# Optimization experiments

Measured on AMD Instinct MI355X. Metric: run time of the kernel, lower is better.

## Reference

```python
import jax, jax.numpy as jnp
import numpy as np

B, N_LATENT, N_NUISANCE, N_OUT = 2048, 64, 16, 2048


def setup_inputs() -> dict:
    key = jax.random.key(0)
    ks = jax.random.split(key, 6)
    z = jax.random.normal(ks[0], (B, N_LATENT + N_NUISANCE), dtype=jnp.float32)
    size_factor = jax.random.uniform(ks[1], (B, 1), dtype=jnp.float32) + 0.5
    # nn.Linear(n_latent, n_out, bias=False): store as [L, O] for z0 @ W
    amat_w = jax.random.normal(ks[2], (N_LATENT, N_OUT), dtype=jnp.float32) / np.sqrt(N_LATENT).astype(np.float32)
    amat_site = jax.random.normal(ks[3], (N_NUISANCE, N_LATENT, N_OUT), dtype=jnp.float32)
    offsets = jax.random.normal(ks[4], (N_NUISANCE, N_OUT), dtype=jnp.float32)
    px_r = jax.random.normal(ks[5], (N_OUT,), dtype=jnp.float32)
    return {"z": z, "size_factor": size_factor, "amat_w": amat_w,
            "amat_site": amat_site, "offsets": offsets, "px_r": px_r}


def reference(z, size_factor, amat_w, amat_site, offsets, px_r):
    n_nuisance = offsets.shape[0]
    nuisance_oh = z[..., -n_nuisance:]          # [B, N] one-hot site indicator
    z0 = z[..., :-n_nuisance]                   # [B, L] latent part
    x1 = z0 @ amat_w                            # [B, O] shared linear decoder
    nuisance_ids = jnp.argmax(nuisance_oh, axis=-1)  # [B] int ids
    # dropout(p=0.1) in eval mode == identity; .detach() -> stop_gradient
    z0_d = jax.lax.stop_gradient(z0)
    As = amat_site[nuisance_ids]                # [B, L, O] per-sample gathered weights
    x2 = jnp.einsum('bl,blo->bo', z0_d, As)     # batched matvec reduction over L
    mu = jax.nn.softmax(x1 + x2 + offsets[nuisance_ids], axis=-1)  # [B, O]
    mu = mu * size_factor                       # scale by per-cell size factor
    theta = jnp.exp(px_r)                       # NB inverse-dispersion, [O]
    return mu, theta
```

## Files before the change

kernel.cpp:

```cpp
#include <hip/hip_runtime.h>
#include <hip/hip_bf16.h>

#define NB 2048
#define NL 64
#define NN 16
#define NROW 80
#define NO 2048
#define TPB 256
#define OPT 8

typedef unsigned int   u32;
typedef unsigned short u16;

__device__ __forceinline__ float bflo(u32 u) { union { u32 i; float f; } c; c.i = u << 16;          return c.f; }
__device__ __forceinline__ float bfhi(u32 u) { union { u32 i; float f; } c; c.i = u & 0xffff0000u;  return c.f; }
__device__ __forceinline__ u16 f2bf(float f) { __hip_bfloat16 h = __float2bfloat16(f); return *(u16*)&h; }

__global__ __launch_bounds__(TPB) void build_m(const float* __restrict__ W,
                                               const float* __restrict__ A,
                                               u16* __restrict__ M) {
    size_t t    = (size_t)blockIdx.x * TPB + threadIdx.x;
    size_t base = t * 4;
    float4 w = *(const float4*)(W + (base & (size_t)(NL * NO - 1)));
    float4 a = *(const float4*)(A + base);
    ushort4 m;
    m.x = f2bf(w.x + a.x);
    m.y = f2bf(w.y + a.y);
    m.z = f2bf(w.z + a.z);
    m.w = f2bf(w.w + a.w);
    *(ushort4*)(M + base) = m;
}

__global__ __launch_bounds__(TPB) void decoder_m(
    const float* __restrict__ z,
    const float* __restrict__ sf,
    const u16*   __restrict__ M,
    const float* __restrict__ offs,
    const float* __restrict__ pxr,
    float* __restrict__ out)
{
    const int b   = blockIdx.x;
    const int tid = threadIdx.x;

    if (b == NB) {
        for (int o = tid; o < NO; o += TPB)
            out[(size_t)NB * NO + o] = __expf(pxr[o]);
        return;
    }

    __shared__ float z0s[NL];
    __shared__ int   s_id;
    __shared__ float s_red[6];

    if (tid < NL) z0s[tid] = z[b * NROW + tid];
    if (tid == 0) {
        float best = -1e30f; int bi = 0;
        for (int i = 0; i < NN; ++i) {
            float v = z[b * NROW + NL + i];
            if (v > best) { best = v; bi = i; }
        }
        s_id = bi;
    }
    __syncthreads();
    const int id = s_id;

    const int o0 = tid * OPT;
    const uint4* mv = (const uint4*)(M + (size_t)id * NL * NO + o0);

    float acc[OPT];
    {
        float4 oa = *(const float4*)(offs + id * NO + o0);
        float4 ob = *(const float4*)(offs + id * NO + o0 + 4);
        acc[0] = oa.x; acc[1] = oa.y; acc[2] = oa.z; acc[3] = oa.w;
        acc[4] = ob.x; acc[5] = ob.y; acc[6] = ob.z; acc[7] = ob.w;
    }

    #pragma unroll 8
    for (int l = 0; l < NL; ++l) {
        const float zl = z0s[l];
        uint4 m = mv[l * (NO / OPT)];
        acc[0] += zl * bflo(m.x); acc[1] += zl * bfhi(m.x);
        acc[2] += zl * bflo(m.y); acc[3] += zl * bfhi(m.y);
        acc[4] += zl * bflo(m.z); acc[5] += zl * bfhi(m.z);
        acc[6] += zl * bflo(m.w); acc[7] += zl * bfhi(m.w);
    }

    float m = acc[0];
    #pragma unroll
    for (int j = 1; j < OPT; ++j) m = fmaxf(m, acc[j]);
    #pragma unroll
    for (int off = 32; off > 0; off >>= 1) m = fmaxf(m, __shfl_down(m, off));
    if ((tid & 63) == 0) s_red[tid >> 6] = m;
    __syncthreads();
    if (tid == 0) s_red[4] = fmaxf(fmaxf(s_red[0], s_red[1]), fmaxf(s_red[2], s_red[3]));
    __syncthreads();
    const float mx = s_red[4];

    float ex[OPT];
    float s = 0.f;
    #pragma unroll
    for (int j = 0; j < OPT; ++j) { ex[j] = __expf(acc[j] - mx); s += ex[j]; }
    #pragma unroll
    for (int off = 32; off > 0; off >>= 1) s += __shfl_down(s, off);
    if ((tid & 63) == 0) s_red[tid >> 6] = s;
    __syncthreads();
    if (tid == 0) s_red[5] = (s_red[0] + s_red[1]) + (s_red[2] + s_red[3]);
    __syncthreads();
    const float scale = sf[b] / s_red[5];

    float* op = out + (size_t)b * NO + o0;
    *(float4*)(op)     = make_float4(ex[0] * scale, ex[1] * scale, ex[2] * scale, ex[3] * scale);
    *(float4*)(op + 4) = make_float4(ex[4] * scale, ex[5] * scale, ex[6] * scale, ex[7] * scale);
}

__global__ __launch_bounds__(TPB) void decoder_f(
    const float* __restrict__ z, const float* __restrict__ sf,
    const float* __restrict__ W, const float* __restrict__ A,
    const float* __restrict__ offs, const float* __restrict__ pxr,
    float* __restrict__ out)
{
    const int b   = blockIdx.x;
    const int tid = threadIdx.x;
    if (b == NB) {
        for (int o = tid; o < NO; o += TPB)
            out[(size_t)NB * NO + o] = __expf(pxr[o]);
        return;
    }
    __shared__ float z0s[NL];
    __shared__ int   s_id;
    __shared__ float s_red[6];
    if (tid < NL) z0s[tid] = z[b * NROW + tid];
    if (tid == 0) {
        float best = -1e30f; int bi = 0;
        for (int i = 0; i < NN; ++i) {
            float v = z[b * NROW + NL + i];
            if (v > best) { best = v; bi = i; }
        }
        s_id = bi;
    }
    __syncthreads();
    const int id = s_id;
    const int o0 = tid * OPT;
    const float* wp = W + o0;
    const float* ap = A + (size_t)id * NL * NO + o0;
    float acc[OPT];
    {
        float4 oa = *(const float4*)(offs + id * NO + o0);
        float4 ob = *(const float4*)(offs + id * NO + o0 + 4);
        acc[0] = oa.x; acc[1] = oa.y; acc[2] = oa.z; acc[3] = oa.w;
        acc[4] = ob.x; acc[5] = ob.y; acc[6] = ob.z; acc[7] = ob.w;
    }
    #pragma unroll 4
    for (int l = 0; l < NL; ++l) {
        const float zl = z0s[l];
        float4 w0 = *(const float4*)(wp + l * NO);
        float4 w1 = *(const float4*)(wp + l * NO + 4);
        float4 a0 = *(const float4*)(ap + l * NO);
        float4 a1 = *(const float4*)(ap + l * NO + 4);
        acc[0] += zl * (w0.x + a0.x); acc[1] += zl * (w0.y + a0.y);
        acc[2] += zl * (w0.z + a0.z); acc[3] += zl * (w0.w + a0.w);
        acc[4] += zl * (w1.x + a1.x); acc[5] += zl * (w1.y + a1.y);
        acc[6] += zl * (w1.z + a1.z); acc[7] += zl * (w1.w + a1.w);
    }
    float m = acc[0];
    #pragma unroll
    for (int j = 1; j < OPT; ++j) m = fmaxf(m, acc[j]);
    #pragma unroll
    for (int off = 32; off > 0; off >>= 1) m = fmaxf(m, __shfl_down(m, off));
    if ((tid & 63) == 0) s_red[tid >> 6] = m;
    __syncthreads();
    if (tid == 0) s_red[4] = fmaxf(fmaxf(s_red[0], s_red[1]), fmaxf(s_red[2], s_red[3]));
    __syncthreads();
    const float mx = s_red[4];
    float ex[OPT];
    float s = 0.f;
    #pragma unroll
    for (int j = 0; j < OPT; ++j) { ex[j] = __expf(acc[j] - mx); s += ex[j]; }
    #pragma unroll
    for (int off = 32; off > 0; off >>= 1) s += __shfl_down(s, off);
    if ((tid & 63) == 0) s_red[tid >> 6] = s;
    __syncthreads();
    if (tid == 0) s_red[5] = (s_red[0] + s_red[1]) + (s_red[2] + s_red[3]);
    __syncthreads();
    const float scale = sf[b] / s_red[5];
    float* op = out + (size_t)b * NO + o0;
    *(float4*)(op)     = make_float4(ex[0] * scale, ex[1] * scale, ex[2] * scale, ex[3] * scale);
    *(float4*)(op + 4) = make_float4(ex[4] * scale, ex[5] * scale, ex[6] * scale, ex[7] * scale);
}

extern "C" void kernel_launch(void* const* d_in, const int* in_sizes, int n_in,
                              void* d_out, int out_size, void* d_ws, size_t ws_size,
                              hipStream_t stream) {
    const float* z    = (const float*)d_in[0];
    const float* sf   = (const float*)d_in[1];
    const float* W    = (const float*)d_in[2];
    const float* A    = (const float*)d_in[3];
    const float* offs = (const float*)d_in[4];
    const float* pxr  = (const float*)d_in[5];
    float* out = (float*)d_out;

    const size_t m_bytes = (size_t)NN * NL * NO * sizeof(u16);
    if (ws_size >= m_bytes) {
        u16* M = (u16*)d_ws;
        hipLaunchKernelGGL(build_m, dim3((NN * NL * NO / 4) / TPB), dim3(TPB), 0, stream, W, A, M);
        hipLaunchKernelGGL(decoder_m, dim3(NB + 1), dim3(TPB), 0, stream, z, sf, M, offs, pxr, out);
    } else {
        hipLaunchKernelGGL(decoder_f, dim3(NB + 1), dim3(TPB), 0, stream, z, sf, W, A, offs, pxr, out);
    }
}
```

Measured before the change: 101.8 us.

## Bucket rows by nuisance id and process groups of eight rows per block

A prep kernel now computes each row's argmax site id, builds per-site row lists with shared-memory atomics, and also does the bf16 weight fold and the theta exp. The decoder launches one block per chunk of eight same-site rows, so each bf16 weight tile load is reused across eight rows instead of one. This cuts weight traffic per output row but raises register pressure (64 accumulators per thread) and launches many empty blocks for sparse buckets. Row order within a bucket depends on atomics, which does not change the results.

```diff
diff --git a/kernel.cpp b/kernel.cpp
--- a/kernel.cpp
+++ b/kernel.cpp
@@ -8,6 +8,9 @@
 #define NO 2048
 #define TPB 256
 #define OPT 8
+#define G 8
+#define CHUNKS (NB / G)
+#define MBLK (NN * NL * NO / 4 / TPB)
 
 typedef unsigned int   u32;
 typedef unsigned short u16;
@@ -16,101 +19,170 @@
 __device__ __forceinline__ float bfhi(u32 u) { union { u32 i; float f; } c; c.i = u & 0xffff0000u;  return c.f; }
 __device__ __forceinline__ u16 f2bf(float f) { __hip_bfloat16 h = __float2bfloat16(f); return *(u16*)&h; }
 
-__global__ __launch_bounds__(TPB) void build_m(const float* __restrict__ W,
-                                               const float* __restrict__ A,
-                                               u16* __restrict__ M) {
-    size_t t    = (size_t)blockIdx.x * TPB + threadIdx.x;
-    size_t base = t * 4;
-    float4 w = *(const float4*)(W + (base & (size_t)(NL * NO - 1)));
-    float4 a = *(const float4*)(A + base);
-    ushort4 m;
-    m.x = f2bf(w.x + a.x);
-    m.y = f2bf(w.y + a.y);
-    m.z = f2bf(w.z + a.z);
-    m.w = f2bf(w.w + a.w);
-    *(ushort4*)(M + base) = m;
-}
-
-__global__ __launch_bounds__(TPB) void decoder_m(
+__global__ __launch_bounds__(TPB) void prep(
+    const float* __restrict__ W,
+    const float* __restrict__ A,
+    const float* __restrict__ z,
+    const float* __restrict__ pxr,
+    u16* __restrict__ M,
+    u32* __restrict__ counts,
+    u32* __restrict__ perm,
+    float* __restrict__ out)
+{
+    const int blk = blockIdx.x;
+    const int tid = threadIdx.x;
+
+    if (blk < MBLK) {
+        size_t t    = (size_t)blk * TPB + tid;
+        size_t base = t * 4;
+        float4 w = *(const float4*)(W + (base & (size_t)(NL * NO - 1)));
+        float4 a = *(const float4*)(A + base);
+        ushort4 m;
+        m.x = f2bf(w.x + a.x);
+        m.y = f2bf(w.y + a.y);
+        m.z = f2bf(w.z + a.z);
+        m.w = f2bf(w.w + a.w);
+        *(ushort4*)(M + base) = m;
+        return;
+    }
+
+    if (blk == MBLK) {
+        __shared__ u32 lc[NN];
+        if (tid < NN) lc[tid] = 0;
+        __syncthreads();
+        #pragma unroll
+        for (int k = 0; k < NB / TPB; ++k) {
+            const int b = k * TPB + tid;
+            const float* zp = z + (size_t)b * NROW + NL;
+            float4 v0 = *(const float4*)(zp);
+            float4 v1 = *(const float4*)(zp + 4);
+            float4 v2 = *(const float4*)(zp + 8);
+            float4 v3 = *(const float4*)(zp + 12);
+            float best = v0.x; int bi = 0;
+            #define CK(val, idx) if ((val) > best) { best = (val); bi = (idx); }
+            CK(v0.y, 1)  CK(v0.z, 2)  CK(v0.w, 3)
+            CK(v1.x, 4)  CK(v1.y, 5)  CK(v1.z, 6)  CK(v1.w, 7)
+            CK(v2.x, 8)  CK(v2.y, 9)  CK(v2.z, 10) CK(v2.w, 11)
+            CK(v3.x, 12) CK(v3.y, 13) CK(v3.z, 14) CK(v3.w, 15)
+            #undef CK
+            u32 pos = atomicAdd(&lc[bi], 1u);
+            perm[(u32)bi * NB + pos] = (u32)b;
+        }
+        __syncthreads();
+        if (tid < NN) counts[tid] = lc[tid];
+        return;
+    }
+
+    for (int o = tid; o < NO; o += TPB)
+        out[(size_t)NB * NO + o] = __expf(pxr[o]);
+}
+
+__global__ __launch_bounds__(TPB) void decoder_g(
     const float* __restrict__ z,
     const float* __restrict__ sf,
     const u16*   __restrict__ M,
     const float* __restrict__ offs,
-    const float* __restrict__ pxr,
+    const u32*   __restrict__ counts,
+    const u32*   __restrict__ perm,
     float* __restrict__ out)
 {
-    const int b   = blockIdx.x;
+    const int bucket = blockIdx.x / CHUNKS;
+    const int chunk  = blockIdx.x % CHUNKS;
+    const u32 cnt    = counts[bucket];
+    if ((u32)(chunk * G) >= cnt) return;
     const int tid = threadIdx.x;
 
-    if (b == NB) {
-        for (int o = tid; o < NO; o += TPB)
-            out[(size_t)NB * NO + o] = __expf(pxr[o]);
-        return;
-    }
-
-    __shared__ float z0s[NL];
-    __shared__ int   s_id;
-    __shared__ float s_red[6];
-
-    if (tid < NL) z0s[tid] = z[b * NROW + tid];
-    if (tid == 0) {
-        float best = -1e30f; int bi = 0;
-        for (int i = 0; i < NN; ++i) {
-            float v = z[b * NROW + NL + i];
-            if (v > best) { best = v; bi = i; }
-        }
-        s_id = bi;
-    }
-    __syncthreads();
-    const int id = s_id;
+    __shared__ float zt[NL][G];
+    __shared__ float s_sf[G];
+    __shared__ u32   s_rows[G];
+    __shared__ float s_red[2][G][4];
+
+    if (tid < G) {
+        u32 idx = (u32)(chunk * G + tid);
+        u32 clamped = idx < cnt ? idx : (cnt - 1u);
+        u32 r = perm[(size_t)bucket * NB + clamped];
+        s_rows[tid] = r;
+        s_sf[tid]   = sf[r];
+    }
+    __syncthreads();
+    {
+        const int l = tid & (NL - 1);
+        const int g = tid >> 6;
+        u32 r0 = s_rows[g], r1 = s_rows[g + 4];
+        zt[l][g]     = z[(size_t)r0 * NROW + l];
+        zt[l][g + 4] = z[(size_t)r1 * NROW + l];
+    }
+    __syncthreads();
 
     const int o0 = tid * OPT;
-    const uint4* mv = (const uint4*)(M + (size_t)id * NL * NO + o0);
-
-    float acc[OPT];
+    const uint4* mv = (const uint4*)(M + (size_t)bucket * (NL * NO) + o0);
+
+    float acc[G][OPT];
     {
-        float4 oa = *(const float4*)(offs + id * NO + o0);
-        float4 ob = *(const float4*)(offs + id * NO + o0 + 4);
-        acc[0] = oa.x; acc[1] = oa.y; acc[2] = oa.z; acc[3] = oa.w;
-        acc[4] = ob.x; acc[5] = ob.y; acc[6] = ob.z; acc[7] = ob.w;
+        float4 oa = *(const float4*)(offs + bucket * NO + o0);
+        float4 ob = *(const float4*)(offs + bucket * NO + o0 + 4);
+        #pragma unroll
+        for (int g = 0; g < G; ++g) {
+            acc[g][0] = oa.x; acc[g][1] = oa.y; acc[g][2] = oa.z; acc[g][3] = oa.w;
+            acc[g][4] = ob.x; acc[g][5] = ob.y; acc[g][6] = ob.z; acc[g][7] = ob.w;
+        }
     }
 
     #pragma unroll 8
     for (int l = 0; l < NL; ++l) {
-        const float zl = z0s[l];
-        uint4 m = mv[l * (NO / OPT)];
-        acc[0] += zl * bflo(m.x); acc[1] += zl * bfhi(m.x);
-        acc[2] += zl * bflo(m.y); acc[3] += zl * bfhi(m.y);
-        acc[4] += zl * bflo(m.z); acc[5] += zl * bfhi(m.z);
-        acc[6] += zl * bflo(m.w); acc[7] += zl * bfhi(m.w);
-    }
-
-    float m = acc[0];
-    #pragma unroll
-    for (int j = 1; j < OPT; ++j) m = fmaxf(m, acc[j]);
-    #pragma unroll
-    for (int off = 32; off > 0; off >>= 1) m = fmaxf(m, __shfl_down(m, off));
-    if ((tid & 63) == 0) s_red[tid >> 6] = m;
-    __syncthreads();
-    if (tid == 0) s_red[4] = fmaxf(fmaxf(s_red[0], s_red[1]), fmaxf(s_red[2], s_red[3]));
-    __syncthreads();
-    const float mx = s_red[4];
-
-    float ex[OPT];
-    float s = 0.f;
-    #pragma unroll
-    for (int j = 0; j < OPT; ++j) { ex[j] = __expf(acc[j] - mx); s += ex[j]; }
-    #pragma unroll
-    for (int off = 32; off > 0; off >>= 1) s += __shfl_down(s, off);
-    if ((tid & 63) == 0) s_red[tid >> 6] = s;
-    __syncthreads();
-    if (tid == 0) s_red[5] = (s_red[0] + s_red[1]) + (s_red[2] + s_red[3]);
-    __syncthreads();
-    const float scale = sf[b] / s_red[5];
-
-    float* op = out + (size_t)b * NO + o0;
-    *(float4*)(op)     = make_float4(ex[0] * scale, ex[1] * scale, ex[2] * scale, ex[3] * scale);
-    *(float4*)(op + 4) = make_float4(ex[4] * scale, ex[5] * scale, ex[6] * scale, ex[7] * scale);
+        const uint4 m = mv[l * (NO / OPT)];
+        float v[OPT];
+        v[0] = bflo(m.x); v[1] = bfhi(m.x);
+        v[2] = bflo(m.y); v[3] = bfhi(m.y);
+        v[4] = bflo(m.z); v[5] = bfhi(m.z);
+        v[6] = bflo(m.w); v[7] = bfhi(m.w);
+        const float4 za = *(const float4*)(&zt[l][0]);
+        const float4 zb = *(const float4*)(&zt[l][4]);
+        const float zg[G] = { za.x, za.y, za.z, za.w, zb.x, zb.y, zb.z, zb.w };
+        #pragma unroll
+        for (int g = 0; g < G; ++g)
+            #pragma unroll
+            for (int j = 0; j < OPT; ++j)
+                acc[g][j] += zg[g] * v[j];
+    }
+
+    const int wv = tid >> 6;
+    #pragma unroll
+    for (int g = 0; g < G; ++g) {
+        float m = acc[g][0];
+        #pragma unroll
+        for (int j = 1; j < OPT; ++j) m = fmaxf(m, acc[g][j]);
+        #pragma unroll
+        for (int off = 32; off > 0; off >>= 1) m = fmaxf(m, __shfl_down(m, off));
+        if ((tid & 63) == 0) s_red[0][g][wv] = m;
+    }
+    __syncthreads();
+    float mx[G];
+    #pragma unroll
+    for (int g = 0; g < G; ++g)
+        mx[g] = fmaxf(fmaxf(s_red[0][g][0], s_red[0][g][1]),
+                      fmaxf(s_red[0][g][2], s_red[0][g][3]));
+
+    #pragma unroll
+    for (int g = 0; g < G; ++g) {
+        float s = 0.f;
+        #pragma unroll
+        for (int j = 0; j < OPT; ++j) { acc[g][j] = __expf(acc[g][j] - mx[g]); s += acc[g][j]; }
+        #pragma unroll
+        for (int off = 32; off > 0; off >>= 1) s += __shfl_down(s, off);
+        if ((tid & 63) == 0) s_red[1][g][wv] = s;
+    }
+    __syncthreads();
+    #pragma unroll
+    for (int g = 0; g < G; ++g) {
+        if ((u32)(chunk * G + g) < cnt) {
+            const float sm  = (s_red[1][g][0] + s_red[1][g][1]) + (s_red[1][g][2] + s_red[1][g][3]);
+            const float scl = s_sf[g] / sm;
+            float* op = out + (size_t)s_rows[g] * NO + o0;
+            *(float4*)(op)     = make_float4(acc[g][0] * scl, acc[g][1] * scl, acc[g][2] * scl, acc[g][3] * scl);
+            *(float4*)(op + 4) = make_float4(acc[g][4] * scl, acc[g][5] * scl, acc[g][6] * scl, acc[g][7] * scl);
+        }
+    }
 }
 
 __global__ __launch_bounds__(TPB) void decoder_f(
@@ -200,11 +272,17 @@
     float* out = (float*)d_out;
 
     const size_t m_bytes = (size_t)NN * NL * NO * sizeof(u16);
-    if (ws_size >= m_bytes) {
-        u16* M = (u16*)d_ws;
-        hipLaunchKernelGGL(build_m, dim3((NN * NL * NO / 4) / TPB), dim3(TPB), 0, stream, W, A, M);
-        hipLaunchKernelGGL(decoder_m, dim3(NB + 1), dim3(TPB), 0, stream, z, sf, M, offs, pxr, out);
+    const size_t need    = m_bytes + 256 + (size_t)NN * NB * sizeof(u32);
+    if (ws_size >= need) {
+        u16* M      = (u16*)d_ws;
+        u32* counts = (u32*)((char*)d_ws + m_bytes);
+        u32* perm   = (u32*)((char*)d_ws + m_bytes + 256);
+        hipLaunchKernelGGL(prep, dim3(MBLK + 2), dim3(TPB), 0, stream,
+                           W, A, z, pxr, M, counts, perm, out);
+        hipLaunchKernelGGL(decoder_g, dim3(NN * CHUNKS), dim3(TPB), 0, stream,
+                           z, sf, M, offs, counts, perm, out);
     } else {
-        hipLaunchKernelGGL(decoder_f, dim3(NB + 1), dim3(TPB), 0, stream, z, sf, W, A, offs, pxr, out);
-    }
-}
+        hipLaunchKernelGGL(decoder_f, dim3(NB + 1), dim3(TPB), 0, stream,
+                           z, sf, W, A, offs, pxr, out);
+    }
+}
```

After: 111.9 us. +9.9%, slower.
